# Performance work log

Hardware: AMD Instinct MI355X
Metric: run time of the kernel (lower is better)

The kernel has to match this reference:

```python
import jax, jax.numpy as jnp
import numpy as np
from jax import lax

FEAT_STRIDE = 16
SCALES = (8.0, 16.0, 32.0)
RATIOS = (0.5, 1.0, 2.0)
PRE_NMS_TOPN = 6000
POST_NMS_TOPN = 300
NMS_THRESH = 0.5
MIN_SIZE = 16.0


def _generate_anchors(base_size=16.0):
    # Faithful Caffe generate_anchors: ratio enumeration outer, scale inner.
    w = h = base_size
    x_ctr = y_ctr = (base_size - 1.0) / 2.0
    size = w * h
    anchors = []
    for r in RATIOS:
        ws = np.round(np.sqrt(size / r))
        hs = np.round(ws * r)
        for s in SCALES:
            W = ws * s
            H = hs * s
            anchors.append([x_ctr - (W - 1) / 2.0, y_ctr - (H - 1) / 2.0,
                            x_ctr + (W - 1) / 2.0, y_ctr + (H - 1) / 2.0])
    return np.asarray(anchors, dtype=np.float32)  # (A=9, 4)


def _nms_keep(boxes, thresh):
    # boxes sorted by descending score; returns bool keep mask. JIT-friendly.
    n = boxes.shape[0]
    x1, y1, x2, y2 = boxes[:, 0], boxes[:, 1], boxes[:, 2], boxes[:, 3]
    areas = (x2 - x1 + 1.0) * (y2 - y1 + 1.0)
    xx1 = jnp.maximum(x1[:, None], x1[None, :])
    yy1 = jnp.maximum(y1[:, None], y1[None, :])
    xx2 = jnp.minimum(x2[:, None], x2[None, :])
    yy2 = jnp.minimum(y2[:, None], y2[None, :])
    inter = jnp.maximum(xx2 - xx1 + 1.0, 0.0) * jnp.maximum(yy2 - yy1 + 1.0, 0.0)
    iou = inter / (areas[:, None] + areas[None, :] - inter)  # (n, n)
    idxs = jnp.arange(n)

    def body(i, keep):
        suppress = (iou[i] > thresh) & keep[i] & (idxs > i)
        return keep & ~suppress

    return lax.fori_loop(0, n, body, jnp.ones((n,), dtype=bool))


def _proposal(scores, bbox_deltas):
    # scores: (1, H, W, 2A) rpn class probs; bbox_deltas: (1, H, W, 4A)
    _, H, W, A4 = bbox_deltas.shape
    A = A4 // 4
    im_h = jnp.float32(H * FEAT_STRIDE)
    im_w = jnp.float32(W * FEAT_STRIDE)

    anchors = jnp.asarray(_generate_anchors())  # (A, 4)
    shift_x = jnp.arange(W, dtype=jnp.float32) * FEAT_STRIDE
    shift_y = jnp.arange(H, dtype=jnp.float32) * FEAT_STRIDE
    sx, sy = jnp.meshgrid(shift_x, shift_y)  # (H, W) row-major like Caffe
    shifts = jnp.stack([sx.ravel(), sy.ravel(), sx.ravel(), sy.ravel()], axis=1)  # (K, 4)
    all_anchors = (anchors[None, :, :] + shifts[:, None, :]).reshape(-1, 4)  # (K*A, 4)

    fg_scores = scores[0, :, :, A:].reshape(-1)        # (K*A,) fg probs
    deltas = bbox_deltas[0].reshape(-1, 4)             # (K*A, 4)

    # bbox_transform_inv (Caffe convention with +1 widths)
    aw = all_anchors[:, 2] - all_anchors[:, 0] + 1.0
    ah = all_anchors[:, 3] - all_anchors[:, 1] + 1.0
    acx = all_anchors[:, 0] + 0.5 * aw
    acy = all_anchors[:, 1] + 0.5 * ah
    dx, dy, dw, dh = deltas[:, 0], deltas[:, 1], deltas[:, 2], deltas[:, 3]
    pcx = dx * aw + acx
    pcy = dy * ah + acy
    pw = jnp.exp(dw) * aw
    ph = jnp.exp(dh) * ah
    x1 = jnp.clip(pcx - 0.5 * pw, 0.0, im_w - 1.0)
    y1 = jnp.clip(pcy - 0.5 * ph, 0.0, im_h - 1.0)
    x2 = jnp.clip(pcx + 0.5 * pw, 0.0, im_w - 1.0)
    y2 = jnp.clip(pcy + 0.5 * ph, 0.0, im_h - 1.0)
    proposals = jnp.stack([x1, y1, x2, y2], axis=1)  # (K*A, 4)

    # min_size filter (im scale = 1): mask score to -inf instead of removing
    ws = x2 - x1 + 1.0
    hs = y2 - y1 + 1.0
    valid = (ws >= MIN_SIZE) & (hs >= MIN_SIZE)
    masked_scores = jnp.where(valid, fg_scores, -jnp.inf)

    top_scores, order = lax.top_k(masked_scores, PRE_NMS_TOPN)
    top_boxes = proposals[order]  # (pre_nms, 4), score-descending

    keep = _nms_keep(lax.stop_gradient(top_boxes), NMS_THRESH)
    keep = keep & jnp.isfinite(top_scores)

    n = PRE_NMS_TOPN
    ranked = jnp.where(keep, jnp.arange(n), n)
    picked = jnp.sort(ranked)[:POST_NMS_TOPN]  # first kept in score order
    ok = picked < n
    picked_c = jnp.minimum(picked, n - 1)
    out_boxes = top_boxes[picked_c] * ok[:, None].astype(top_boxes.dtype)

    # normalized proposals in [0, 1]
    scale = jnp.array([im_w, im_h, im_w, im_h], dtype=top_boxes.dtype)
    return out_boxes / scale  # (post_nms_topN, 4)


def setup_inputs() -> dict:
    key = jax.random.key(0)
    k1, k2 = jax.random.split(key)
    scores = jax.random.uniform(k1, (1, 64, 64, 18), dtype=jnp.float32)
    bbox_deltas = jax.random.normal(k2, (1, 64, 64, 36), dtype=jnp.float32)
    return {"scores": scores, "bbox_deltas": bbox_deltas}


def reference(scores, bbox_deltas):
    return _proposal(scores, bbox_deltas)
```

## Files before the change

### kernel.cpp

```cpp
#include <hip/hip_runtime.h>
#include <math.h>


#define NPROP   36864
#define TOPN    6000
#define POSTN   300
#define NWORDS  94
#define NROUND  47
#define MAXSEL  8192
#define NB      16384
#define SPLIT   8
#define NEGINF_PAT 0x007FFFFFu

typedef unsigned long long u64;

__constant__ float ANCH[9][4] = {
    {-84.f,  -40.f,  99.f,  55.f},
    {-176.f, -88.f,  191.f, 103.f},
    {-360.f, -184.f, 375.f, 199.f},
    {-56.f,  -56.f,  71.f,  71.f},
    {-120.f, -120.f, 135.f, 135.f},
    {-248.f, -248.f, 263.f, 263.f},
    {-36.f,  -80.f,  51.f,  95.f},
    {-80.f,  -168.f, 95.f,  183.f},
    {-168.f, -344.f, 183.f, 359.f},
};

__device__ __forceinline__ float4 decode_box(const float* __restrict__ deltas, int i,
                                             bool* valid_out) {
    int a   = i % 9;
    int pos = i / 9;
    int wx = pos & 63, hy = pos >> 6;
    float sx = (float)(wx * 16), sy = (float)(hy * 16);
    float ax1 = ANCH[a][0] + sx, ay1 = ANCH[a][1] + sy;
    float ax2 = ANCH[a][2] + sx, ay2 = ANCH[a][3] + sy;
    float aw  = ax2 - ax1 + 1.0f;
    float ah  = ay2 - ay1 + 1.0f;
    float acx = ax1 + 0.5f * aw;
    float acy = ay1 + 0.5f * ah;
    float4 d4 = ((const float4*)deltas)[i];
    float pcx = __fadd_rn(__fmul_rn(d4.x, aw), acx);
    float pcy = __fadd_rn(__fmul_rn(d4.y, ah), acy);
    float pw  = __fmul_rn(expf(d4.z), aw);
    float ph  = __fmul_rn(expf(d4.w), ah);
    float hx  = __fmul_rn(0.5f, pw);
    float hv  = __fmul_rn(0.5f, ph);
    float x1 = fminf(fmaxf(__fsub_rn(pcx, hx), 0.0f), 1023.0f);
    float y1 = fminf(fmaxf(__fsub_rn(pcy, hv), 0.0f), 1023.0f);
    float x2 = fminf(fmaxf(__fadd_rn(pcx, hx), 0.0f), 1023.0f);
    float y2 = fminf(fmaxf(__fadd_rn(pcy, hv), 0.0f), 1023.0f);
    float bw = __fadd_rn(__fsub_rn(x2, x1), 1.0f);
    float bh = __fadd_rn(__fsub_rn(y2, y1), 1.0f);
    *valid_out = (bw >= 16.0f) && (bh >= 16.0f);
    return make_float4(x1, y1, x2, y2);
}

__device__ __forceinline__ float box_area(float4 b) {
    return __fmul_rn(__fadd_rn(__fsub_rn(b.z, b.x), 1.0f),
                     __fadd_rn(__fsub_rn(b.w, b.y), 1.0f));
}

__global__ __launch_bounds__(256) void decode_kernel(
        const float* __restrict__ scores,
        const float* __restrict__ deltas,
        unsigned* __restrict__ uhigh,
        unsigned* __restrict__ ghist) {
    __shared__ unsigned h[NB];
    int t = threadIdx.x;
    #pragma unroll
    for (int r = 0; r < NB / 256; ++r) h[t + r * 256] = 0;
    __syncthreads();

    int i = blockIdx.x * 256 + t;
    bool valid;
    (void)decode_box(deltas, i, &valid);
    int a = i % 9, pos = i / 9;
    float fg = scores[(size_t)pos * 18 + 9 + a];
    float sc = valid ? fg : -__builtin_huge_valf();
    unsigned u = __float_as_uint(sc);
    u = (u & 0x80000000u) ? ~u : (u | 0x80000000u);
    uhigh[i] = u;
    atomicAdd(&h[u >> 18], 1u);
    __syncthreads();

    #pragma unroll
    for (int r = 0; r < NB / 256; ++r) {
        unsigned v = h[t + r * 256];
        if (v) atomicAdd(&ghist[t + r * 256], v);
    }
}

__global__ __launch_bounds__(1024) void select_compact(
        const unsigned* __restrict__ ghist,
        const unsigned* __restrict__ uhigh,
        u64* __restrict__ sel,
        unsigned* __restrict__ nsel) {
    __shared__ unsigned strip[1024];
    __shared__ unsigned thr_sh, cnt_sh;
    int t = threadIdx.x, lane = t & 63, wave = t >> 6;

    const uint4* g4 = (const uint4*)ghist;
    uint4 qa = g4[t * 4 + 0], qb = g4[t * 4 + 1], qc = g4[t * 4 + 2], qd = g4[t * 4 + 3];
    unsigned s = qa.x + qa.y + qa.z + qa.w + qb.x + qb.y + qb.z + qb.w
               + qc.x + qc.y + qc.z + qc.w + qd.x + qd.y + qd.z + qd.w;
    strip[t] = s;
    if (t == 0) cnt_sh = 0;
    __syncthreads();

    if (wave == 0) {
        unsigned g = 0;
        #pragma unroll
        for (int k = 0; k < 16; ++k) g += strip[lane * 16 + k];
        unsigned suf = g;
        #pragma unroll
        for (int off = 1; off < 64; off <<= 1) {
            unsigned x = __shfl_down(suf, off, 64);
            if (lane + off < 64) suf += x;
        }
        u64 bal = __ballot(suf >= TOPN);
        int gsel = 63 - __builtin_clzll(bal);
        unsigned rest = __shfl(suf, (gsel < 63) ? gsel + 1 : 63, 64);
        if (gsel == 63) rest = 0;

        unsigned sv = (lane < 16) ? strip[gsel * 16 + lane] : 0;
        unsigned suf2 = sv;
        #pragma unroll
        for (int off = 1; off < 16; off <<= 1) {
            unsigned x = __shfl_down(suf2, off, 64);
            if (lane + off < 16) suf2 += x;
        }
        u64 bal2 = __ballot((lane < 16) && (rest + suf2 >= TOPN));
        int ssel = 63 - __builtin_clzll(bal2);
        unsigned rest2 = __shfl(suf2, (ssel < 15) ? ssel + 1 : 15, 64);
        if (ssel == 15) rest2 = 0;
        rest2 += rest;
        int S = gsel * 16 + ssel;

        unsigned bv = (lane < 16) ? ghist[S * 16 + lane] : 0;
        unsigned suf3 = bv;
        #pragma unroll
        for (int off = 1; off < 16; off <<= 1) {
            unsigned x = __shfl_down(suf3, off, 64);
            if (lane + off < 16) suf3 += x;
        }
        u64 bal3 = __ballot((lane < 16) && (rest2 + suf3 >= TOPN));
        int bsel = 63 - __builtin_clzll(bal3);
        if (lane == 0) thr_sh = ((unsigned)(S * 16 + bsel)) << 18;
    }
    __syncthreads();
    unsigned thr = thr_sh;

    for (int r = 0; r < 36; ++r) {
        unsigned u = uhigh[t + r * 1024];
        bool pred = (u >= thr);
        u64 b = __ballot(pred);
        int nb = __popcll(b);
        unsigned base = 0;
        if (lane == 0 && nb) base = atomicAdd(&cnt_sh, (unsigned)nb);
        base = __shfl(base, 0, 64);
        if (pred) {
            unsigned p = base + (unsigned)__popcll(b & ((1ULL << lane) - 1ULL));
            if (p < MAXSEL)
                sel[p] = ((u64)u << 32) |
                         (u64)(0xFFFFFFFFu - (unsigned)(t + r * 1024));
        }
    }
    __syncthreads();
    if (t == 0) *nsel = (cnt_sh > MAXSEL) ? MAXSEL : cnt_sh;
}

__global__ __launch_bounds__(256) void rank_partial(
        const u64* __restrict__ sel,
        const unsigned* __restrict__ nsel,
        int* __restrict__ rank8) {
    __shared__ u64 tile[1024];
    int t = threadIdx.x;
    int j = blockIdx.x * 256 + t;
    int n = (int)*nsel;
    int T = (n + SPLIT - 1) / SPLIT;
    int lo = blockIdx.y * T;
    int hi = min(lo + T, n);
    u64 myk = (j < n) ? sel[j] : 0ULL;
    int rk = 0;
    for (int base = lo; base < hi; base += 1024) {
        int m = min(1024, hi - base);
        for (int q = t; q < m; q += 256) tile[q] = sel[base + q];
        __syncthreads();
        #pragma unroll 4
        for (int q = 0; q < m; ++q) rk += (tile[q] > myk) ? 1 : 0;
        __syncthreads();
    }
    rank8[blockIdx.y * MAXSEL + j] = rk;
}

__global__ __launch_bounds__(256) void scatter_top(
        const u64* __restrict__ sel,
        const unsigned* __restrict__ nsel,
        const int* __restrict__ rank8,
        const float* __restrict__ deltas,
        float4* __restrict__ topb,
        float* __restrict__ areas,
        unsigned* __restrict__ topu) {
    int j = blockIdx.x * 256 + threadIdx.x;
    int n = (int)*nsel;
    if (j >= n) return;
    int r = 0;
    #pragma unroll
    for (int s = 0; s < SPLIT; ++s) r += rank8[s * MAXSEL + j];
    if (r >= TOPN) return;
    u64 k = sel[j];
    unsigned idx = 0xFFFFFFFFu - (unsigned)(k & 0xFFFFFFFFull);
    bool valid;
    float4 b = decode_box(deltas, (int)idx, &valid);
    topb[r] = b;
    areas[r] = box_area(b);
    topu[r] = (unsigned)(k >> 32);
}

__global__ void nms_mask(const float4* __restrict__ boxes,
                         const float* __restrict__ areas,
                         u64* __restrict__ mask) {
    int rb = blockIdx.x, cb = blockIdx.y;
    if (cb < rb) return;
    __shared__ float4 cbx[64];
    __shared__ float  car[64];
    int tid = threadIdx.x;
    int j0 = cb * 64;
    if (j0 + tid < TOPN) { cbx[tid] = boxes[j0 + tid]; car[tid] = areas[j0 + tid]; }
    __syncthreads();
    int i = rb * 64 + tid;
    if (i >= TOPN) return;
    float4 bi = boxes[i];
    float  ai = areas[i];
    u64 bits = 0ULL;
    int jmax = min(64, TOPN - j0);
    for (int jj = 0; jj < jmax; ++jj) {
        int j = j0 + jj;
        if (j <= i) continue;
        float4 bj = cbx[jj];
        float xx1 = fmaxf(bi.x, bj.x);
        float yy1 = fmaxf(bi.y, bj.y);
        float xx2 = fminf(bi.z, bj.z);
        float yy2 = fminf(bi.w, bj.w);
        float w = fmaxf(__fadd_rn(__fsub_rn(xx2, xx1), 1.0f), 0.0f);
        float h = fmaxf(__fadd_rn(__fsub_rn(yy2, yy1), 1.0f), 0.0f);
        float inter = __fmul_rn(w, h);
        float denom = __fsub_rn(__fadd_rn(ai, car[jj]), inter);
        float iou = inter / denom;
        if (iou > 0.5f) bits |= (1ULL << jj);
    }
    mask[(size_t)i * NWORDS + cb] = bits;
}

__global__ __launch_bounds__(1024) void nms_scan(
        const u64* __restrict__ mask,
        const unsigned* __restrict__ topu,
        const float4* __restrict__ topb,
        float* __restrict__ out) {
    __shared__ unsigned rem32[NWORDS * 2];
    __shared__ u64 diag[2][128][4];
    __shared__ u64 Fsh[2][2];
    __shared__ short kept_rows[2][128];
    __shared__ short kept_list[POSTN];
    __shared__ int nk_sh[2];
    __shared__ int cnt_sh, stop_sh;

    int t = threadIdx.x, wave = t >> 6, lane = t & 63;
    if (t >= 640 && t < 640 + NWORDS * 2) rem32[t - 640] = 0;
    if (t >= 128 && t < 640) {
        int idx = t - 128;
        diag[0][idx >> 2][idx & 3] = mask[(size_t)(idx >> 2) * NWORDS + (idx & 3)];
    }
    if (wave == 0) {
        u64 f = __ballot(topu[lane] != NEGINF_PAT);
        if (lane == 0) { Fsh[0][0] = f; cnt_sh = 0; stop_sh = 0; nk_sh[0] = 0; nk_sh[1] = 0; }
    } else if (wave == 1) {
        u64 f = __ballot(topu[64 + lane] != NEGINF_PAT);
        if (lane == 0) Fsh[0][1] = f;
    }
    __syncthreads();

    u64 urg0 = 0, urg1 = 0;

    for (int r = 0; r < NROUND; ++r) {
        int p = r & 1;
        int i0 = r * 128;
        if (wave == 0) {
            u64 r0w0 = diag[p][lane][0];
            u64 r0w1 = diag[p][lane][1];
            u64 r1w1 = diag[p][64 + lane][1];
            u64 R0 = ((u64)rem32[4 * r]     | ((u64)rem32[4 * r + 1] << 32)) | urg0;
            u64 R1 = ((u64)rem32[4 * r + 2] | ((u64)rem32[4 * r + 3] << 32)) | urg1;
            int nb = min(128, TOPN - i0);
            u64 v1 = (nb >= 128) ? ~0ULL : ((1ULL << (nb - 64)) - 1ULL);
            u64 a0 = ~R0;
            u64 a1 = ~R1 & v1;
            u64 k0 = 0ULL, k1 = 0ULL;
            while (a0) {
                int ii = __builtin_ctzll(a0);
                u64 bit = 1ULL << ii;
                k0 |= bit;
                u64 s0 = __shfl(r0w0, ii, 64);
                u64 s1 = __shfl(r0w1, ii, 64);
                a0 &= ~(s0 | bit);
                a1 &= ~s1;
            }
            while (a1) {
                int ii = __builtin_ctzll(a1);
                u64 bit = 1ULL << ii;
                k1 |= bit;
                u64 s1 = __shfl(r1w1, ii, 64);
                a1 &= ~(s1 | bit);
            }
            u64 F0 = Fsh[p][0], F1 = Fsh[p][1];
            u64 kf0 = k0 & F0, kf1 = k1 & F1;
            int nk0 = __popcll(k0);
            int c0  = __popcll(kf0);
            int base = cnt_sh;
            u64 ltm = (1ULL << lane) - 1ULL;
            if ((k0 >> lane) & 1)
                kept_rows[p][__popcll(k0 & ltm)] = (short)(i0 + lane);
            if ((k1 >> lane) & 1)
                kept_rows[p][nk0 + __popcll(k1 & ltm)] = (short)(i0 + 64 + lane);
            if ((kf0 >> lane) & 1) {
                int pos = base + __popcll(kf0 & ltm);
                if (pos < POSTN) kept_list[pos] = (short)(i0 + lane);
            }
            if ((kf1 >> lane) & 1) {
                int pos = base + c0 + __popcll(kf1 & ltm);
                if (pos < POSTN) kept_list[pos] = (short)(i0 + 64 + lane);
            }
            u64 a0u = 0ULL, a1u = 0ULL;
            if ((k0 >> lane) & 1) { a0u = diag[p][lane][2];       a1u = diag[p][lane][3]; }
            if ((k1 >> lane) & 1) { a0u |= diag[p][64 + lane][2]; a1u |= diag[p][64 + lane][3]; }
            #pragma unroll
            for (int off = 1; off < 64; off <<= 1) {
                a0u |= __shfl_xor(a0u, off, 64);
                a1u |= __shfl_xor(a1u, off, 64);
            }
            urg0 = a0u; urg1 = a1u;
            if (lane == 0) {
                nk_sh[p] = nk0 + __popcll(k1);
                int cc = base + c0 + __popcll(kf1);
                if (cc > POSTN) cc = POSTN;
                cnt_sh = cc;
                stop_sh = (cc >= POSTN) || (r == NROUND - 1);
            }
        } else if (wave == 15) {
            if (r + 1 < NROUND) {
                int i1 = i0 + 128;
                #pragma unroll
                for (int q = lane; q < 512; q += 64) {
                    int row = i1 + (q >> 2), k = q & 3;
                    int wd = 2 * (r + 1) + k;
                    diag[p ^ 1][q >> 2][k] = (row < TOPN && wd < NWORDS)
                        ? mask[(size_t)row * NWORDS + wd] : 0ULL;
                }
                u64 fa = __ballot((i1 + lane < TOPN) && (topu[i1 + lane] != NEGINF_PAT));
                u64 fb = __ballot((i1 + 64 + lane < TOPN) && (topu[i1 + 64 + lane] != NEGINF_PAT));
                if (lane == 0) { Fsh[p ^ 1][0] = fa; Fsh[p ^ 1][1] = fb; }
            }
        } else {
            int nkp = nk_sh[p ^ 1];
            int left = NWORDS - (2 * r + 2);
            if (r > 0 && nkp > 0 && left > 0) {
                int tot = nkp * left;
                for (int q = t - 64; q < tot; q += 896) {
                    int k  = q / left;
                    int wd = 2 * r + 2 + (q - k * left);
                    int row = kept_rows[p ^ 1][k];
                    u64 v = mask[(size_t)row * NWORDS + wd];
                    if (v) {
                        unsigned lo = (unsigned)v, hi = (unsigned)(v >> 32);
                        if (lo) atomicOr(&rem32[2 * wd],     lo);
                        if (hi) atomicOr(&rem32[2 * wd + 1], hi);
                    }
                }
            }
        }
        __syncthreads();
        if (stop_sh) break;
    }

    if (t < POSTN) {
        float4 v = make_float4(0.f, 0.f, 0.f, 0.f);
        if (t < cnt_sh) {
            float4 b = topb[kept_list[t]];
            const float s = 0.0009765625f;
            v = make_float4(b.x * s, b.y * s, b.z * s, b.w * s);
        }
        ((float4*)out)[t] = v;
    }
}

extern "C" void kernel_launch(void* const* d_in, const int* in_sizes, int n_in,
                              void* d_out, int out_size, void* d_ws, size_t ws_size,
                              hipStream_t stream) {
    const float* scores = (const float*)d_in[0];
    const float* deltas = (const float*)d_in[1];
    float* out = (float*)d_out;

    char* w = (char*)d_ws;
    unsigned* uhigh = (unsigned*)(w);
    u64*      sel   = (u64*)(w + 147456);
    unsigned* nsel  = (unsigned*)(w + 212992);
    int*      rank8 = (int*)(w + 213008);
    float4*   topb  = (float4*)(w + 475152);
    float*    areas = (float*)(w + 571152);
    unsigned* topu  = (unsigned*)(w + 595152);
    unsigned* ghist = (unsigned*)(w + 619152);
    u64*      mask  = (u64*)(w + 684688);

    hipMemsetAsync(ghist, 0, NB * sizeof(unsigned), stream);
    decode_kernel<<<NPROP / 256, 256, 0, stream>>>(scores, deltas, uhigh, ghist);
    select_compact<<<1, 1024, 0, stream>>>(ghist, uhigh, sel, nsel);
    rank_partial<<<dim3(MAXSEL / 256, SPLIT), 256, 0, stream>>>(sel, nsel, rank8);
    scatter_top<<<MAXSEL / 256, 256, 0, stream>>>(sel, nsel, rank8, deltas, topb, areas, topu);
    nms_mask<<<dim3(NWORDS, NWORDS), 64, 0, stream>>>(topb, areas, mask);
    nms_scan<<<1, 1024, 0, stream>>>(mask, topu, topb, out);
}
```

Baseline: 153.0 us.

## Build histogram in select kernel and fuse rank with scatter

The global histogram, its memset and the per-block shared histograms are dropped from the decode kernel. The single-block select kernel now builds the whole 16K-bin histogram in shared memory, using a transposed layout so that each thread's 16-bin strip sums without extra passes. The separate rank and scatter kernels are merged into one kernel: each block ranks 32 keys, with 8 segments splitting the comparisons, and the scatter happens after a shared-memory reduction. This removes one memset, one launch and the rank8 round trip through global memory. In exchange the 36K-element histogram is built by one block instead of many, and the rank kernel now runs 256 blocks, each scanning all selected keys.

```diff
diff --git a/kernel.cpp b/kernel.cpp
--- a/kernel.cpp
+++ b/kernel.cpp
@@ -9,7 +9,6 @@
 #define NROUND  47
 #define MAXSEL  8192
 #define NB      16384
-#define SPLIT   8
 #define NEGINF_PAT 0x007FFFFFu
 
 typedef unsigned long long u64;
@@ -63,15 +62,8 @@
 __global__ __launch_bounds__(256) void decode_kernel(
         const float* __restrict__ scores,
         const float* __restrict__ deltas,
-        unsigned* __restrict__ uhigh,
-        unsigned* __restrict__ ghist) {
-    __shared__ unsigned h[NB];
-    int t = threadIdx.x;
-    #pragma unroll
-    for (int r = 0; r < NB / 256; ++r) h[t + r * 256] = 0;
-    __syncthreads();
-
-    int i = blockIdx.x * 256 + t;
+        unsigned* __restrict__ uhigh) {
+    int i = blockIdx.x * 256 + threadIdx.x;
     bool valid;
     (void)decode_box(deltas, i, &valid);
     int a = i % 9, pos = i / 9;
@@ -80,31 +72,33 @@
     unsigned u = __float_as_uint(sc);
     u = (u & 0x80000000u) ? ~u : (u | 0x80000000u);
     uhigh[i] = u;
-    atomicAdd(&h[u >> 18], 1u);
-    __syncthreads();
-
-    #pragma unroll
-    for (int r = 0; r < NB / 256; ++r) {
-        unsigned v = h[t + r * 256];
-        if (v) atomicAdd(&ghist[t + r * 256], v);
-    }
 }
 
 __global__ __launch_bounds__(1024) void select_compact(
-        const unsigned* __restrict__ ghist,
         const unsigned* __restrict__ uhigh,
         u64* __restrict__ sel,
         unsigned* __restrict__ nsel) {
+    __shared__ unsigned h[NB];
     __shared__ unsigned strip[1024];
     __shared__ unsigned thr_sh, cnt_sh;
     int t = threadIdx.x, lane = t & 63, wave = t >> 6;
-
-    const uint4* g4 = (const uint4*)ghist;
-    uint4 qa = g4[t * 4 + 0], qb = g4[t * 4 + 1], qc = g4[t * 4 + 2], qd = g4[t * 4 + 3];
-    unsigned s = qa.x + qa.y + qa.z + qa.w + qb.x + qb.y + qb.z + qb.w
-               + qc.x + qc.y + qc.z + qc.w + qd.x + qd.y + qd.z + qd.w;
+    #pragma unroll
+    for (int r = 0; r < NB / 1024; ++r) h[t + r * 1024] = 0;
+    if (t == 0) cnt_sh = 0;
+    __syncthreads();
+
+    #pragma unroll
+    for (int r = 0; r < 36; ++r) {
+        unsigned u = uhigh[t + r * 1024];
+        unsigned bkt = u >> 18;
+        atomicAdd(&h[(bkt >> 4) + (bkt & 15) * 1024], 1u);
+    }
+    __syncthreads();
+
+    unsigned s = 0;
+    #pragma unroll
+    for (int k = 0; k < 16; ++k) s += h[t + k * 1024];
     strip[t] = s;
-    if (t == 0) cnt_sh = 0;
     __syncthreads();
 
     if (wave == 0) {
@@ -136,7 +130,7 @@
         rest2 += rest;
         int S = gsel * 16 + ssel;
 
-        unsigned bv = (lane < 16) ? ghist[S * 16 + lane] : 0;
+        unsigned bv = (lane < 16) ? h[S + lane * 1024] : 0;
         unsigned suf3 = bv;
         #pragma unroll
         for (int off = 1; off < 16; off <<= 1) {
@@ -169,52 +163,45 @@
     if (t == 0) *nsel = (cnt_sh > MAXSEL) ? MAXSEL : cnt_sh;
 }
 
-__global__ __launch_bounds__(256) void rank_partial(
+__global__ __launch_bounds__(256) void rank_scatter(
         const u64* __restrict__ sel,
         const unsigned* __restrict__ nsel,
-        int* __restrict__ rank8) {
-    __shared__ u64 tile[1024];
-    int t = threadIdx.x;
-    int j = blockIdx.x * 256 + t;
-    int n = (int)*nsel;
-    int T = (n + SPLIT - 1) / SPLIT;
-    int lo = blockIdx.y * T;
-    int hi = min(lo + T, n);
-    u64 myk = (j < n) ? sel[j] : 0ULL;
-    int rk = 0;
-    for (int base = lo; base < hi; base += 1024) {
-        int m = min(1024, hi - base);
-        for (int q = t; q < m; q += 256) tile[q] = sel[base + q];
-        __syncthreads();
-        #pragma unroll 4
-        for (int q = 0; q < m; ++q) rk += (tile[q] > myk) ? 1 : 0;
-        __syncthreads();
-    }
-    rank8[blockIdx.y * MAXSEL + j] = rk;
-}
-
-__global__ __launch_bounds__(256) void scatter_top(
-        const u64* __restrict__ sel,
-        const unsigned* __restrict__ nsel,
-        const int* __restrict__ rank8,
         const float* __restrict__ deltas,
         float4* __restrict__ topb,
         float* __restrict__ areas,
         unsigned* __restrict__ topu) {
-    int j = blockIdx.x * 256 + threadIdx.x;
-    int n = (int)*nsel;
-    if (j >= n) return;
-    int r = 0;
-    #pragma unroll
-    for (int s = 0; s < SPLIT; ++s) r += rank8[s * MAXSEL + j];
-    if (r >= TOPN) return;
-    u64 k = sel[j];
-    unsigned idx = 0xFFFFFFFFu - (unsigned)(k & 0xFFFFFFFFull);
-    bool valid;
-    float4 b = decode_box(deltas, (int)idx, &valid);
-    topb[r] = b;
-    areas[r] = box_area(b);
-    topu[r] = (unsigned)(k >> 32);
+    __shared__ u64 tile[1024];
+    __shared__ int pr[256];
+    int t = threadIdx.x;
+    int slot = t & 31, seg = t >> 5;
+    int n = (int)*nsel; if (n > MAXSEL) n = MAXSEL;
+    int j = blockIdx.x * 32 + slot;
+    u64 myk = (j < n) ? sel[j] : 0ULL;
+    int rk = 0;
+    for (int base = 0; base < n; base += 1024) {
+        int m = min(1024, n - base);
+        for (int q = t; q < m; q += 256) tile[q] = sel[base + q];
+        __syncthreads();
+        for (int q = seg; q < m; q += 8) rk += (tile[q] > myk) ? 1 : 0;
+        __syncthreads();
+    }
+    pr[seg * 32 + slot] = rk;
+    __syncthreads();
+    if (t < 32) {
+        int jj = blockIdx.x * 32 + t;
+        int rtot = 0;
+        #pragma unroll
+        for (int s2 = 0; s2 < 8; ++s2) rtot += pr[s2 * 32 + t];
+        if (jj < n && rtot < TOPN) {
+            u64 k = sel[jj];
+            unsigned idx = 0xFFFFFFFFu - (unsigned)(k & 0xFFFFFFFFull);
+            bool valid;
+            float4 b = decode_box(deltas, (int)idx, &valid);
+            topb[rtot]  = b;
+            areas[rtot] = box_area(b);
+            topu[rtot]  = (unsigned)(k >> 32);
+        }
+    }
 }
 
 __global__ void nms_mask(const float4* __restrict__ boxes,
@@ -404,18 +391,14 @@
     unsigned* uhigh = (unsigned*)(w);
     u64*      sel   = (u64*)(w + 147456);
     unsigned* nsel  = (unsigned*)(w + 212992);
-    int*      rank8 = (int*)(w + 213008);
-    float4*   topb  = (float4*)(w + 475152);
-    float*    areas = (float*)(w + 571152);
-    unsigned* topu  = (unsigned*)(w + 595152);
-    unsigned* ghist = (unsigned*)(w + 619152);
-    u64*      mask  = (u64*)(w + 684688);
-
-    hipMemsetAsync(ghist, 0, NB * sizeof(unsigned), stream);
-    decode_kernel<<<NPROP / 256, 256, 0, stream>>>(scores, deltas, uhigh, ghist);
-    select_compact<<<1, 1024, 0, stream>>>(ghist, uhigh, sel, nsel);
-    rank_partial<<<dim3(MAXSEL / 256, SPLIT), 256, 0, stream>>>(sel, nsel, rank8);
-    scatter_top<<<MAXSEL / 256, 256, 0, stream>>>(sel, nsel, rank8, deltas, topb, areas, topu);
+    float4*   topb  = (float4*)(w + 213008);
+    float*    areas = (float*)(w + 309008);
+    unsigned* topu  = (unsigned*)(w + 333008);
+    u64*      mask  = (u64*)(w + 357008);
+
+    decode_kernel<<<NPROP / 256, 256, 0, stream>>>(scores, deltas, uhigh);
+    select_compact<<<1, 1024, 0, stream>>>(uhigh, sel, nsel);
+    rank_scatter<<<MAXSEL / 32, 256, 0, stream>>>(sel, nsel, deltas, topb, areas, topu);
     nms_mask<<<dim3(NWORDS, NWORDS), 64, 0, stream>>>(topb, areas, mask);
     nms_scan<<<1, 1024, 0, stream>>>(mask, topu, topb, out);
 }
```

Result: slower. 175.6 us (+14.8%).

## Build score histogram inside single-block select kernel instead of global atomics

Applied to the files above, without the earlier changes.

Moves the 16K-bucket radix histogram out of the decode kernel (per-block shared histogram plus global atomic flush) into the single-block select kernel. That kernel now reads all uhigh values itself and builds the histogram in shared memory with a transposed bucket layout. This removes the memset launch, the 144 blocks each zeroing and flushing 16K shared bins, and the global atomics. In exchange, one 1024-thread block must now process all 36864 entries serially, with 64KB of LDS for the histogram.

```diff
diff --git a/kernel.cpp b/kernel.cpp
--- a/kernel.cpp
+++ b/kernel.cpp
@@ -63,15 +63,8 @@
 __global__ __launch_bounds__(256) void decode_kernel(
         const float* __restrict__ scores,
         const float* __restrict__ deltas,
-        unsigned* __restrict__ uhigh,
-        unsigned* __restrict__ ghist) {
-    __shared__ unsigned h[NB];
-    int t = threadIdx.x;
-    #pragma unroll
-    for (int r = 0; r < NB / 256; ++r) h[t + r * 256] = 0;
-    __syncthreads();
-
-    int i = blockIdx.x * 256 + t;
+        unsigned* __restrict__ uhigh) {
+    int i = blockIdx.x * 256 + threadIdx.x;
     bool valid;
     (void)decode_box(deltas, i, &valid);
     int a = i % 9, pos = i / 9;
@@ -80,31 +73,33 @@
     unsigned u = __float_as_uint(sc);
     u = (u & 0x80000000u) ? ~u : (u | 0x80000000u);
     uhigh[i] = u;
-    atomicAdd(&h[u >> 18], 1u);
-    __syncthreads();
-
-    #pragma unroll
-    for (int r = 0; r < NB / 256; ++r) {
-        unsigned v = h[t + r * 256];
-        if (v) atomicAdd(&ghist[t + r * 256], v);
-    }
 }
 
 __global__ __launch_bounds__(1024) void select_compact(
-        const unsigned* __restrict__ ghist,
         const unsigned* __restrict__ uhigh,
         u64* __restrict__ sel,
         unsigned* __restrict__ nsel) {
+    __shared__ unsigned h[NB];
     __shared__ unsigned strip[1024];
     __shared__ unsigned thr_sh, cnt_sh;
     int t = threadIdx.x, lane = t & 63, wave = t >> 6;
-
-    const uint4* g4 = (const uint4*)ghist;
-    uint4 qa = g4[t * 4 + 0], qb = g4[t * 4 + 1], qc = g4[t * 4 + 2], qd = g4[t * 4 + 3];
-    unsigned s = qa.x + qa.y + qa.z + qa.w + qb.x + qb.y + qb.z + qb.w
-               + qc.x + qc.y + qc.z + qc.w + qd.x + qd.y + qd.z + qd.w;
+    #pragma unroll
+    for (int r = 0; r < NB / 1024; ++r) h[t + r * 1024] = 0;
+    if (t == 0) cnt_sh = 0;
+    __syncthreads();
+
+    #pragma unroll
+    for (int r = 0; r < 36; ++r) {
+        unsigned u = uhigh[t + r * 1024];
+        unsigned bkt = u >> 18;
+        atomicAdd(&h[(bkt >> 4) + (bkt & 15) * 1024], 1u);
+    }
+    __syncthreads();
+
+    unsigned s = 0;
+    #pragma unroll
+    for (int k = 0; k < 16; ++k) s += h[t + k * 1024];
     strip[t] = s;
-    if (t == 0) cnt_sh = 0;
     __syncthreads();
 
     if (wave == 0) {
@@ -136,7 +131,7 @@
         rest2 += rest;
         int S = gsel * 16 + ssel;
 
-        unsigned bv = (lane < 16) ? ghist[S * 16 + lane] : 0;
+        unsigned bv = (lane < 16) ? h[S + lane * 1024] : 0;
         unsigned suf3 = bv;
         #pragma unroll
         for (int off = 1; off < 16; off <<= 1) {
@@ -212,9 +207,9 @@
     unsigned idx = 0xFFFFFFFFu - (unsigned)(k & 0xFFFFFFFFull);
     bool valid;
     float4 b = decode_box(deltas, (int)idx, &valid);
-    topb[r] = b;
+    topb[r]  = b;
     areas[r] = box_area(b);
-    topu[r] = (unsigned)(k >> 32);
+    topu[r]  = (unsigned)(k >> 32);
 }
 
 __global__ void nms_mask(const float4* __restrict__ boxes,
@@ -408,12 +403,10 @@
     float4*   topb  = (float4*)(w + 475152);
     float*    areas = (float*)(w + 571152);
     unsigned* topu  = (unsigned*)(w + 595152);
-    unsigned* ghist = (unsigned*)(w + 619152);
-    u64*      mask  = (u64*)(w + 684688);
-
-    hipMemsetAsync(ghist, 0, NB * sizeof(unsigned), stream);
-    decode_kernel<<<NPROP / 256, 256, 0, stream>>>(scores, deltas, uhigh, ghist);
-    select_compact<<<1, 1024, 0, stream>>>(ghist, uhigh, sel, nsel);
+    u64*      mask  = (u64*)(w + 619152);
+
+    decode_kernel<<<NPROP / 256, 256, 0, stream>>>(scores, deltas, uhigh);
+    select_compact<<<1, 1024, 0, stream>>>(uhigh, sel, nsel);
     rank_partial<<<dim3(MAXSEL / 256, SPLIT), 256, 0, stream>>>(sel, nsel, rank8);
     scatter_top<<<MAXSEL / 256, 256, 0, stream>>>(sel, nsel, rank8, deltas, topb, areas, topu);
     nms_mask<<<dim3(NWORDS, NWORDS), 64, 0, stream>>>(topb, areas, mask);
```

Result: no change. 150.3 us (-1.7%).
